# Performance work log

Hardware: AMD Instinct MI355X
Metric: run time of the kernel (lower is better)

Reference implementation:

```python
import jax, jax.numpy as jnp
import numpy as np

N_NODES = 100000
N_EDGES = 3200000
D_FEAT = 128
UNITS = 128
EPS = 0.0


def setup_inputs() -> dict:
    key = jax.random.key(0)
    k1, k2, k3, k4, k5 = jax.random.split(key, 5)
    X = jax.random.normal(k1, (N_NODES, D_FEAT), dtype=jnp.float32)
    ref_A = jax.random.randint(k2, (N_EDGES,), 0, N_NODES, dtype=jnp.int32)  # dst per edge
    ref_B = jax.random.randint(k3, (N_EDGES,), 0, N_NODES, dtype=jnp.int32)  # src per edge
    # Glorot-uniform weights, zero biases (as in build())
    lim1 = float(np.sqrt(6.0 / (D_FEAT + UNITS)))
    lim2 = float(np.sqrt(6.0 / (UNITS + UNITS)))
    w1 = jax.random.uniform(k4, (D_FEAT, UNITS), minval=-lim1, maxval=lim1, dtype=jnp.float32)
    b1 = jnp.zeros((UNITS,), dtype=jnp.float32)
    w2 = jax.random.uniform(k5, (UNITS, UNITS), minval=-lim2, maxval=lim2, dtype=jnp.float32)
    b2 = jnp.zeros((UNITS,), dtype=jnp.float32)
    return {"X": X, "ref_A": ref_A, "ref_B": ref_B, "w1": w1, "b1": b1, "w2": w2, "b2": b2}


def reference(X, ref_A, ref_B, w1, b1, w2, b2):
    # c.convolution: gather source-node features and scatter-add to destinations
    agg = jax.ops.segment_sum(X[ref_B], ref_A, num_segments=N_NODES)  # [N, d]
    conv_X = (1.0 + EPS) * X + agg
    h = jax.nn.relu(conv_X @ w1 + b1)  # [N, units]
    out = jax.nn.relu(h @ w2 + b2)     # [N, units]
    return out
```

## Files before the change

kernel.cpp:

```cpp
#include <hip/hip_runtime.h>
#include <hip/hip_bf16.h>

#define NNODES 100000
#define DFEAT 128
#define NBKT 8
#define STRIPE 12500
#define BUCKET_CAP 416000
#define CHUNK 4096
#define NSUB 49
#define SUBCAP 9216
#define NSB (NBKT * NSUB)

typedef short bf16x8 __attribute__((ext_vector_type(8)));
typedef float f32x4  __attribute__((ext_vector_type(4)));

__device__ __forceinline__ unsigned short f2bf(float f) {
    unsigned u = __builtin_bit_cast(unsigned, f);
    return (unsigned short)((u + 0x7fffu + ((u >> 16) & 1u)) >> 16);
}

__global__ __launch_bounds__(256)
void x2bf_kernel(const float4* __restrict__ X, uint4* __restrict__ Xb, int n8) {
    int i = blockIdx.x * 256 + threadIdx.x;
    if (i >= n8) return;
    float4 a = X[2 * i], b = X[2 * i + 1];
    uint4 o;
    o.x = f2bf(a.x) | ((unsigned)f2bf(a.y) << 16);
    o.y = f2bf(a.z) | ((unsigned)f2bf(a.w) << 16);
    o.z = f2bf(b.x) | ((unsigned)f2bf(b.y) << 16);
    o.w = f2bf(b.z) | ((unsigned)f2bf(b.w) << 16);
    Xb[i] = o;
}

__global__ __launch_bounds__(256)
void wprep(const float* __restrict__ w1, const float* __restrict__ w2,
           unsigned short* __restrict__ w1t, unsigned short* __restrict__ w2t) {
    int i = blockIdx.x * 256 + threadIdx.x;
    const float* w = (i < 16384) ? w1 : w2;
    unsigned short* o = (i < 16384) ? w1t : w2t;
    int j = i & 16383;
    int n = j >> 7, k = j & 127;
    o[n * 128 + k] = f2bf(w[k * 128 + n]);
}

__global__ __launch_bounds__(256)
void partition_edges(const int* __restrict__ dst, const int* __restrict__ src,
                     int* __restrict__ bcur, unsigned* __restrict__ bedges,
                     int nE) {
    __shared__ unsigned sbuf[CHUNK];
    __shared__ int scnt[NBKT];
    __shared__ int sbase[NBKT];
    __shared__ int scur[NBKT];
    __shared__ int gbase[NBKT];

    const int tid = threadIdx.x;
    const long long e0 = (long long)blockIdx.x * CHUNK;
    const int n = (int)min((long long)CHUNK, (long long)nE - e0);
    if (n <= 0) return;

    if (tid < NBKT) scnt[tid] = 0;
    __syncthreads();

    unsigned ent[CHUNK / 256];
    int bkt[CHUNK / 256];
#pragma unroll
    for (int j = 0; j < CHUNK / 256; ++j) {
        int i = tid + j * 256;
        if (i < n) {
            int d = dst[e0 + i];
            int s = src[e0 + i];
            int b = d / STRIPE;
            ent[j] = (unsigned)s | ((unsigned)(d - b * STRIPE) << 17);
            bkt[j] = b;
            atomicAdd(&scnt[b], 1);
        } else bkt[j] = -1;
    }
    __syncthreads();

    if (tid == 0) {
        int run = 0;
        for (int b = 0; b < NBKT; ++b) { sbase[b] = run; scur[b] = run; run += scnt[b]; }
    }
    __syncthreads();

#pragma unroll
    for (int j = 0; j < CHUNK / 256; ++j)
        if (bkt[j] >= 0) {
            int p = atomicAdd(&scur[bkt[j]], 1);
            sbuf[p] = ent[j];
        }
    if (tid < NBKT) gbase[tid] = atomicAdd(&bcur[tid], scnt[tid]);
    __syncthreads();

    for (int i = tid; i < n; i += 256) {
        int b = 0;
        while (b < NBKT - 1 && i >= sbase[b + 1]) ++b;
        bedges[(size_t)b * BUCKET_CAP + gbase[b] + (i - sbase[b])] = sbuf[i];
    }
}

__global__ __launch_bounds__(256)
void partition_sub(const unsigned* __restrict__ bedges, const int* __restrict__ bcur,
                   int* __restrict__ scur2, unsigned* __restrict__ sub_edges) {
    __shared__ unsigned sbuf[CHUNK];
    __shared__ int scnt[NSUB];
    __shared__ int sbase[NSUB + 1];
    __shared__ int scur[NSUB];
    __shared__ int gbase[NSUB];

    const int b   = blockIdx.x & (NBKT - 1);
    const int blk = blockIdx.x >> 3;
    const int sz  = bcur[b];
    const int e0  = blk * CHUNK;
    if (e0 >= sz) return;
    const int n = min(CHUNK, sz - e0);
    const unsigned* p = bedges + (size_t)b * BUCKET_CAP + e0;
    const int tid = threadIdx.x;

    for (int i = tid; i < NSUB; i += 256) scnt[i] = 0;
    __syncthreads();

    unsigned ent[CHUNK / 256];
    int sbk[CHUNK / 256];
#pragma unroll
    for (int j = 0; j < CHUNK / 256; ++j) {
        int i = tid + j * 256;
        if (i < n) {
            unsigned v = p[i];
            int s = (int)(v >> 25);
            ent[j] = v;
            sbk[j] = s;
            atomicAdd(&scnt[s], 1);
        } else sbk[j] = -1;
    }
    __syncthreads();

    if (tid == 0) {
        int run = 0;
        for (int s = 0; s < NSUB; ++s) { sbase[s] = run; scur[s] = run; run += scnt[s]; }
        sbase[NSUB] = run;
    }
    __syncthreads();

#pragma unroll
    for (int j = 0; j < CHUNK / 256; ++j)
        if (sbk[j] >= 0) {
            int pos = atomicAdd(&scur[sbk[j]], 1);
            sbuf[pos] = ent[j];
        }
    if (tid < NSUB) gbase[tid] = atomicAdd(&scur2[b * NSUB + tid], scnt[tid]);
    __syncthreads();

    for (int s = 0; s < NSUB; ++s) {
        int lo = sbase[s], hi = sbase[s + 1];
        int g0 = gbase[s];
        unsigned* q = sub_edges + (size_t)(b * NSUB + s) * SUBCAP;
        for (int i = lo + tid; i < hi; i += 256) {
            int o = g0 + (i - lo);
            if (o < SUBCAP) q[o] = sbuf[i];
        }
    }
}

__device__ __forceinline__ void bfadd(float* acc, uint4 v) {
    acc[0] += __builtin_bit_cast(float, v.x << 16);
    acc[1] += __builtin_bit_cast(float, v.x & 0xffff0000u);
    acc[2] += __builtin_bit_cast(float, v.y << 16);
    acc[3] += __builtin_bit_cast(float, v.y & 0xffff0000u);
    acc[4] += __builtin_bit_cast(float, v.z << 16);
    acc[5] += __builtin_bit_cast(float, v.z & 0xffff0000u);
    acc[6] += __builtin_bit_cast(float, v.w << 16);
    acc[7] += __builtin_bit_cast(float, v.w & 0xffff0000u);
}

__global__ __launch_bounds__(256)
void sort_aggregate(const unsigned* __restrict__ sub_edges,
                    const int* __restrict__ scur2,
                    const uint4* __restrict__ Xb, uint4* __restrict__ convb) {
    __shared__ unsigned srt[SUBCAP];
    __shared__ int cnt[256];
    __shared__ int off[257];
    __shared__ int cur[256];
    __shared__ int tmp[256];

    const int b  = blockIdx.x & (NBKT - 1);
    const int j  = blockIdx.x >> 3;
    const int sb = b * NSUB + j;
    const int tid = threadIdx.x;
    const int sz = min(scur2[sb], SUBCAP);
    const int nodeBase = b * STRIPE + j * 256;
    const int nLoc = min(256, STRIPE - j * 256);
    const unsigned* p = sub_edges + (size_t)sb * SUBCAP;

    cnt[tid] = 0;
    __syncthreads();
    for (int i = tid; i < sz; i += 256)
        atomicAdd(&cnt[(p[i] >> 17) & 255], 1);
    __syncthreads();

    tmp[tid] = cnt[tid];
    __syncthreads();
    for (int d = 1; d < 256; d <<= 1) {
        int t = (tid >= d) ? tmp[tid - d] : 0;
        __syncthreads();
        tmp[tid] += t;
        __syncthreads();
    }
    off[tid + 1] = tmp[tid];
    if (tid == 0) off[0] = 0;
    __syncthreads();
    cur[tid] = off[tid];
    __syncthreads();

    for (int i = tid; i < sz; i += 256) {
        unsigned v = p[i];
        int pos = atomicAdd(&cur[(v >> 17) & 255], 1);
        srt[pos] = v & 0x1FFFFu;
    }
    __syncthreads();

    const int grp = tid >> 4, lane = tid & 15;
    for (int n0 = grp; n0 < nLoc; n0 += 16) {
        int node = nodeBase + n0;
        float acc[8];
#pragma unroll
        for (int q = 0; q < 8; ++q) acc[q] = 0.f;
        bfadd(acc, Xb[(size_t)node * 16 + lane]);

        int e = off[n0], end = off[n0 + 1];
        for (; e + 4 <= end; e += 4) {
            int s0 = srt[e + 0], s1 = srt[e + 1], s2 = srt[e + 2], s3 = srt[e + 3];
            uint4 v0 = Xb[(size_t)s0 * 16 + lane];
            uint4 v1 = Xb[(size_t)s1 * 16 + lane];
            uint4 v2 = Xb[(size_t)s2 * 16 + lane];
            uint4 v3 = Xb[(size_t)s3 * 16 + lane];
            bfadd(acc, v0); bfadd(acc, v1); bfadd(acc, v2); bfadd(acc, v3);
        }
        for (; e < end; ++e)
            bfadd(acc, Xb[(size_t)srt[e] * 16 + lane]);

        uint4 o;
        o.x = f2bf(acc[0]) | ((unsigned)f2bf(acc[1]) << 16);
        o.y = f2bf(acc[2]) | ((unsigned)f2bf(acc[3]) << 16);
        o.z = f2bf(acc[4]) | ((unsigned)f2bf(acc[5]) << 16);
        o.w = f2bf(acc[6]) | ((unsigned)f2bf(acc[7]) << 16);
        convb[(size_t)node * 16 + lane] = o;
    }
}

#define TM 128

__global__ __launch_bounds__(256, 1)
void mlp_fused(const unsigned short* __restrict__ convb,
               const unsigned short* __restrict__ w1t, const float* __restrict__ b1,
               const unsigned short* __restrict__ w2t, const float* __restrict__ b2,
               float* __restrict__ out, int N) {
    __shared__ unsigned short sA[TM][136];
    __shared__ unsigned short sW[128][136];
    __shared__ unsigned short sH[TM][136];

    const int tid  = threadIdx.x;
    const int row0 = blockIdx.x * TM;

    for (int i = tid; i < TM * 16; i += 256) {
        int r = i >> 4, c = i & 15;
        uint4 v = make_uint4(0, 0, 0, 0);
        if (row0 + r < N) v = ((const uint4*)convb)[(size_t)(row0 + r) * 16 + c];
        *(uint4*)&sA[r][c * 8] = v;
    }
    for (int i = tid; i < 128 * 16; i += 256) {
        int r = i >> 4, c = i & 15;
        *(uint4*)&sW[r][c * 8] = ((const uint4*)w1t)[r * 16 + c];
    }
    __syncthreads();

    const int lane = tid & 63;
    const int lrow = lane & 15;
    const int kgrp = lane >> 4;
    const int m0   = (tid >> 6) * 32;

    float bias[8];
#pragma unroll
    for (int nf = 0; nf < 8; ++nf) bias[nf] = b1[nf * 16 + lrow];

    f32x4 acc[2][8] = {};
#pragma unroll
    for (int kk = 0; kk < 128; kk += 32) {
        bf16x8 a0 = *(const bf16x8*)&sA[m0 + lrow][kk + kgrp * 8];
        bf16x8 a1 = *(const bf16x8*)&sA[m0 + 16 + lrow][kk + kgrp * 8];
#pragma unroll
        for (int nf = 0; nf < 8; ++nf) {
            bf16x8 b = *(const bf16x8*)&sW[nf * 16 + lrow][kk + kgrp * 8];
            acc[0][nf] = __builtin_amdgcn_mfma_f32_16x16x32_bf16(a0, b, acc[0][nf], 0, 0, 0);
            acc[1][nf] = __builtin_amdgcn_mfma_f32_16x16x32_bf16(a1, b, acc[1][nf], 0, 0, 0);
        }
    }

#pragma unroll
    for (int mf = 0; mf < 2; ++mf)
#pragma unroll
        for (int nf = 0; nf < 8; ++nf)
#pragma unroll
            for (int r = 0; r < 4; ++r) {
                int row = m0 + mf * 16 + kgrp * 4 + r;
                int col = nf * 16 + lrow;
                float h = fmaxf(acc[mf][nf][r] + bias[nf], 0.f);
                sH[row][col] = f2bf(h);
            }

    __syncthreads();

    for (int i = tid; i < 128 * 16; i += 256) {
        int r = i >> 4, c = i & 15;
        *(uint4*)&sW[r][c * 8] = ((const uint4*)w2t)[r * 16 + c];
    }
#pragma unroll
    for (int nf = 0; nf < 8; ++nf) bias[nf] = b2[nf * 16 + lrow];
#pragma unroll
    for (int mf = 0; mf < 2; ++mf)
#pragma unroll
        for (int nf = 0; nf < 8; ++nf) acc[mf][nf] = (f32x4){0.f, 0.f, 0.f, 0.f};
    __syncthreads();

#pragma unroll
    for (int kk = 0; kk < 128; kk += 32) {
        bf16x8 a0 = *(const bf16x8*)&sH[m0 + lrow][kk + kgrp * 8];
        bf16x8 a1 = *(const bf16x8*)&sH[m0 + 16 + lrow][kk + kgrp * 8];
#pragma unroll
        for (int nf = 0; nf < 8; ++nf) {
            bf16x8 b = *(const bf16x8*)&sW[nf * 16 + lrow][kk + kgrp * 8];
            acc[0][nf] = __builtin_amdgcn_mfma_f32_16x16x32_bf16(a0, b, acc[0][nf], 0, 0, 0);
            acc[1][nf] = __builtin_amdgcn_mfma_f32_16x16x32_bf16(a1, b, acc[1][nf], 0, 0, 0);
        }
    }

#pragma unroll
    for (int mf = 0; mf < 2; ++mf)
#pragma unroll
        for (int nf = 0; nf < 8; ++nf)
#pragma unroll
            for (int r = 0; r < 4; ++r) {
                int row = row0 + m0 + mf * 16 + kgrp * 4 + r;
                int col = nf * 16 + lrow;
                if (row < N)
                    out[(size_t)row * 128 + col] = fmaxf(acc[mf][nf][r] + bias[nf], 0.f);
            }
}

extern "C" void kernel_launch(void* const* d_in, const int* in_sizes, int n_in,
                              void* d_out, int out_size, void* d_ws, size_t ws_size,
                              hipStream_t stream) {
    const float* X    = (const float*)d_in[0];
    const int*   refA = (const int*)d_in[1];
    const int*   refB = (const int*)d_in[2];
    const float* w1   = (const float*)d_in[3];
    const float* b1   = (const float*)d_in[4];
    const float* w2   = (const float*)d_in[5];
    const float* b2   = (const float*)d_in[6];
    float* out = (float*)d_out;

    const int nNodes = in_sizes[0] / DFEAT;
    const int nE     = in_sizes[1];

    char* ws = (char*)d_ws;
    unsigned short* Xb    = (unsigned short*)ws;  ws += (size_t)nNodes * DFEAT * 2;
    unsigned short* convb = (unsigned short*)ws;
    unsigned* bedges      = (unsigned*)convb;
    ws += (size_t)nNodes * DFEAT * 2;
    unsigned* sub_edges = (unsigned*)ws;          ws += (size_t)NSB * SUBCAP * 4;
    unsigned short* w1t = (unsigned short*)ws;    ws += 16384 * 2;
    unsigned short* w2t = (unsigned short*)ws;    ws += 16384 * 2;
    int* bcur  = (int*)ws;                        ws += 64 * 4;
    int* scur2 = (int*)ws;

    int n8 = nNodes * DFEAT / 8;
    x2bf_kernel<<<(n8 + 255) / 256, 256, 0, stream>>>((const float4*)X, (uint4*)Xb, n8);
    wprep<<<128, 256, 0, stream>>>(w1, w2, w1t, w2t);

    hipMemsetAsync(bcur, 0, (64 + NSB) * 4, stream);
    int pBlocks = (nE + CHUNK - 1) / CHUNK;
    partition_edges<<<pBlocks, 256, 0, stream>>>(refA, refB, bcur, bedges, nE);
    partition_sub<<<(BUCKET_CAP / CHUNK + 1) * NBKT, 256, 0, stream>>>(
        bedges, bcur, scur2, sub_edges);

    sort_aggregate<<<NSB, 256, 0, stream>>>(sub_edges, scur2,
                                            (const uint4*)Xb, (uint4*)convb);

    int mBlocks = (nNodes + TM - 1) / TM;
    mlp_fused<<<mBlocks, 256, 0, stream>>>(convb, w1t, b1, w2t, b2, out, nNodes);
}
```

Baseline: 237.9 us.

## Shrink aggregation sub-buckets to 64 nodes and use wave-shuffle prefix scan

Splits each bucket stripe into 196 sub-buckets of 64 destination nodes instead of 49 of 256. This shrinks per-block shared memory and raises launch bounds so more blocks fit per CU. The 256-entry block-wide LDS scan with many barriers becomes a single-wavefront shuffle scan. More, smaller blocks add launch overhead, and the tighter per-sub-bucket capacity raises the risk of overflow truncation on skewed degree distributions.

Measured after the change: 252.2 us. 6.0% more time.

```diff
diff --git a/kernel.cpp b/kernel.cpp
--- a/kernel.cpp
+++ b/kernel.cpp
@@ -7,8 +7,9 @@
 #define STRIPE 12500
 #define BUCKET_CAP 416000
 #define CHUNK 4096
-#define NSUB 49
-#define SUBCAP 9216
+#define SUBNODES 64
+#define NSUB 196
+#define SUBCAP 2560
 #define NSB (NBKT * NSUB)
 
 typedef short bf16x8 __attribute__((ext_vector_type(8)));
@@ -127,7 +128,7 @@
         int i = tid + j * 256;
         if (i < n) {
             unsigned v = p[i];
-            int s = (int)(v >> 25);
+            int s = (int)(v >> 23);
             ent[j] = v;
             sbk[j] = s;
             atomicAdd(&scnt[s], 1);
@@ -173,48 +174,47 @@
     acc[7] += __builtin_bit_cast(float, v.w & 0xffff0000u);
 }
 
-__global__ __launch_bounds__(256)
+__global__ __launch_bounds__(256, 8)
 void sort_aggregate(const unsigned* __restrict__ sub_edges,
                     const int* __restrict__ scur2,
                     const uint4* __restrict__ Xb, uint4* __restrict__ convb) {
     __shared__ unsigned srt[SUBCAP];
-    __shared__ int cnt[256];
-    __shared__ int off[257];
-    __shared__ int cur[256];
-    __shared__ int tmp[256];
+    __shared__ int cnt[SUBNODES];
+    __shared__ int off[SUBNODES + 1];
+    __shared__ int cur[SUBNODES];
 
     const int b  = blockIdx.x & (NBKT - 1);
     const int j  = blockIdx.x >> 3;
     const int sb = b * NSUB + j;
     const int tid = threadIdx.x;
     const int sz = min(scur2[sb], SUBCAP);
-    const int nodeBase = b * STRIPE + j * 256;
-    const int nLoc = min(256, STRIPE - j * 256);
+    const int nodeBase = b * STRIPE + j * SUBNODES;
+    const int nLoc = min(SUBNODES, STRIPE - j * SUBNODES);
     const unsigned* p = sub_edges + (size_t)sb * SUBCAP;
 
-    cnt[tid] = 0;
+    if (tid < SUBNODES) cnt[tid] = 0;
     __syncthreads();
     for (int i = tid; i < sz; i += 256)
-        atomicAdd(&cnt[(p[i] >> 17) & 255], 1);
-    __syncthreads();
-
-    tmp[tid] = cnt[tid];
-    __syncthreads();
-    for (int d = 1; d < 256; d <<= 1) {
-        int t = (tid >= d) ? tmp[tid - d] : 0;
-        __syncthreads();
-        tmp[tid] += t;
-        __syncthreads();
-    }
-    off[tid + 1] = tmp[tid];
-    if (tid == 0) off[0] = 0;
-    __syncthreads();
-    cur[tid] = off[tid];
+        atomicAdd(&cnt[(p[i] >> 17) & 63], 1);
+    __syncthreads();
+
+    if (tid < 64) {
+        int v = cnt[tid];
+        int s = v;
+#pragma unroll
+        for (int d = 1; d < 64; d <<= 1) {
+            int t = __shfl_up(s, d, 64);
+            if (tid >= d) s += t;
+        }
+        off[tid + 1] = s;
+        cur[tid] = s - v;
+        if (tid == 0) off[0] = 0;
+    }
     __syncthreads();
 
     for (int i = tid; i < sz; i += 256) {
         unsigned v = p[i];
-        int pos = atomicAdd(&cur[(v >> 17) & 255], 1);
+        int pos = atomicAdd(&cur[(v >> 17) & 63], 1);
         srt[pos] = v & 0x1FFFFu;
     }
     __syncthreads();
```
